# Kernel optimization log

Measured on AMD Instinct MI355X. Metric: run time of the kernel, lower is better.

Reference implementation:

```python
import jax, jax.numpy as jnp
import numpy as np

D_MODEL = 1024
D_QK = 1024
NUM_HEADS = 16
HEAD_DIM = D_QK // NUM_HEADS      # 64
V_DIM = D_MODEL // NUM_HEADS      # 64
B, S = 2, 2048


def setup_inputs() -> dict:
    key = jax.random.key(0)
    ks = jax.random.split(key, 9)
    sc = 0.02
    return {
        "x": jax.random.normal(ks[0], (B, S, D_MODEL), dtype=jnp.float32),
        "Wqk": jax.random.normal(ks[1], (D_MODEL, 2 * D_QK), dtype=jnp.float32) * sc,
        "bqk": jax.random.normal(ks[2], (2 * D_QK,), dtype=jnp.float32) * sc,
        "Wv": jax.random.normal(ks[3], (D_MODEL, D_MODEL), dtype=jnp.float32) * sc,
        "bv": jax.random.normal(ks[4], (D_MODEL,), dtype=jnp.float32) * sc,
        "Wn": jax.random.normal(ks[5], (D_MODEL, NUM_HEADS), dtype=jnp.float32) * sc,
        "bn": jax.random.normal(ks[6], (NUM_HEADS,), dtype=jnp.float32) * sc,
        "Wo": jax.random.normal(ks[7], (D_MODEL, D_MODEL), dtype=jnp.float32) * sc,
        "bo": jax.random.normal(ks[8], (D_MODEL,), dtype=jnp.float32) * sc,
    }


def reference(x, Wqk, bqk, Wv, bv, Wn, bn, Wo, bo):
    b, s, _ = x.shape
    qk = x @ Wqk + bqk                                  # (B,S,2*D_QK)
    v = x @ Wv + bv                                     # (B,S,D_MODEL)
    n = x @ Wn + bn                                     # (B,S,H)

    qk = qk.reshape(b, s, 2, NUM_HEADS, HEAD_DIM)
    q, k = qk[:, :, 0], qk[:, :, 1]                     # (B,S,H,Dh)
    v = v.reshape(b, s, NUM_HEADS, V_DIM)               # (B,S,H,Dv)

    scores = jnp.einsum('bthd,bshd->bhts', q, k)        # (B,H,S,S)
    mask = jnp.tril(jnp.ones((s, s), dtype=scores.dtype))
    n_exp = jnp.exp(jnp.transpose(n, (0, 2, 1)))        # (B,H,S)
    attn = scores * mask / n_exp[:, :, :, None]         # dropout p=0 (eval)

    ctx = jnp.einsum('bhts,bshd->bthd', attn, v)        # (B,S,H,Dv)
    ctx = ctx.reshape(b, s, D_MODEL)
    return ctx @ Wo + bo
```

## Files before the change

kernel.cpp:

```cpp
#include <hip/hip_runtime.h>
#include <hip/hip_bf16.h>

constexpr int Bb   = 2;
constexpr int Ss   = 2048;
constexpr int Dm   = 1024;
constexpr int Hh   = 16;
constexpr int Hd   = 64;
constexpr int Mtot = Bb * Ss;
constexpr int NCH  = Ss / 64;

typedef __bf16 bf16x8 __attribute__((ext_vector_type(8)));
typedef float  f32x4  __attribute__((ext_vector_type(4)));
typedef __attribute__((address_space(1))) unsigned int u32_as1;
typedef __attribute__((address_space(3))) unsigned int u32_as3;

__device__ __forceinline__ void gload_lds16(const void* g, void* l) {
  __builtin_amdgcn_global_load_lds((const u32_as1*)g, (u32_as3*)l, 16, 0, 0);
}

__device__ __forceinline__ unsigned short f2bf(float f) {
  union { float f; unsigned u; } x; x.f = f;
  unsigned r = x.u + 0x7fffu + ((x.u >> 16) & 1u);
  return (unsigned short)(r >> 16);
}

__device__ __forceinline__ float bf2f(unsigned short s) {
  union { unsigned u; float f; } x; x.u = ((unsigned)s) << 16;
  return x.f;
}

__global__ void k_transpose_conv(const float* __restrict__ W, unsigned short* __restrict__ Wt,
                                 int K, int N) {
  __shared__ float t[32][33];
  int n0 = blockIdx.x * 32, k0 = blockIdx.y * 32;
  int tx = threadIdx.x, ty = threadIdx.y;
#pragma unroll
  for (int j = 0; j < 32; j += 8)
    t[ty + j][tx] = W[(size_t)(k0 + ty + j) * N + n0 + tx];
  __syncthreads();
#pragma unroll
  for (int j = 0; j < 32; j += 8)
    Wt[(size_t)(n0 + ty + j) * K + k0 + tx] = f2bf(t[tx][ty + j]);
}

__global__ void k_n_proj(const float* __restrict__ x, const float* __restrict__ Wn,
                         const float* __restrict__ bn, float* __restrict__ invn,
                         unsigned short* __restrict__ xb) {
  __shared__ float xl[4][1024];
  int tid = threadIdx.x, w = tid >> 6, lane = tid & 63;
  int row = blockIdx.x * 4 + w;
  const float4* x4 = (const float4*)(x + (size_t)row * Dm);
  ushort4* xb4 = (ushort4*)(xb + (size_t)row * Dm);
#pragma unroll
  for (int j = 0; j < 4; ++j) {
    float4 v = x4[j * 64 + lane];
    *(float4*)&xl[w][(j * 64 + lane) * 4] = v;
    ushort4 o;
    o.x = f2bf(v.x); o.y = f2bf(v.y); o.z = f2bf(v.z); o.w = f2bf(v.w);
    xb4[j * 64 + lane] = o;
  }
  __syncthreads();
  const float4* Wn4 = (const float4*)Wn;
  f32x4 sum = {0.f, 0.f, 0.f, 0.f};
#pragma unroll 4
  for (int j = 0; j < 64; ++j) {
    float xv = xl[w][j * 16 + (lane >> 2)];
    float4 wv = Wn4[j * 64 + lane];
    sum[0] += xv * wv.x; sum[1] += xv * wv.y; sum[2] += xv * wv.z; sum[3] += xv * wv.w;
  }
#pragma unroll
  for (int m = 4; m < 64; m <<= 1) {
    sum[0] += __shfl_xor(sum[0], m);
    sum[1] += __shfl_xor(sum[1], m);
    sum[2] += __shfl_xor(sum[2], m);
    sum[3] += __shfl_xor(sum[3], m);
  }
  if (lane < 4) {
    int b = row >> 11, s = row & 2047;
#pragma unroll
    for (int e = 0; e < 4; ++e) {
      int h = lane * 4 + e;
      float nv = sum[e] + bn[h];
      invn[((size_t)(b * Hh + h)) * Ss + s] = expf(-nv);
    }
  }
}

template <int MODE>
__global__ __launch_bounds__(256, 2) void k_gemm_bt(
    const unsigned short* __restrict__ A, const unsigned short* __restrict__ BT,
    const float* __restrict__ bias0, const float* __restrict__ bias1,
    void* __restrict__ out0, void* __restrict__ out1, void* __restrict__ out2,
    void* __restrict__ out3, int M, int N, int K) {
  __shared__ __align__(16) unsigned short As[128 * 64];
  __shared__ __align__(16) unsigned short Bs[128 * 64];
  int tid = threadIdx.x, w = tid >> 6, lane = tid & 63;
  int m0 = blockIdx.y * 128, n0 = blockIdx.x * 128;
  int wm = w >> 1, wn = w & 1;
  f32x4 acc[4][4] = {};

  for (int kt = 0; kt < (K >> 6); ++kt) {
#pragma unroll
    for (int i = 0; i < 4; ++i) {
      int lin = i * 2048 + w * 512 + lane * 8;
      int r = lin >> 6, c = lin & 63;
      gload_lds16(A + (size_t)(m0 + r) * K + kt * 64 + c, As + i * 2048 + w * 512);
    }
#pragma unroll
    for (int i = 0; i < 4; ++i) {
      int lin = i * 2048 + w * 512 + lane * 8;
      int r = lin >> 6, c = lin & 63;
      gload_lds16(BT + (size_t)(n0 + r) * K + kt * 64 + c, Bs + i * 2048 + w * 512);
    }
    __syncthreads();
#pragma unroll
    for (int ks = 0; ks < 2; ++ks) {
      bf16x8 af[4], bfr[4];
#pragma unroll
      for (int mt = 0; mt < 4; ++mt)
        af[mt] = *(const bf16x8*)(As + (wm * 64 + mt * 16 + (lane & 15)) * 64 + ks * 32 + (lane >> 4) * 8);
#pragma unroll
      for (int nt = 0; nt < 4; ++nt)
        bfr[nt] = *(const bf16x8*)(Bs + (wn * 64 + nt * 16 + (lane & 15)) * 64 + ks * 32 + (lane >> 4) * 8);
#pragma unroll
      for (int mt = 0; mt < 4; ++mt)
#pragma unroll
        for (int nt = 0; nt < 4; ++nt)
          acc[mt][nt] = __builtin_amdgcn_mfma_f32_16x16x32_bf16(af[mt], bfr[nt], acc[mt][nt], 0, 0, 0);
    }
    __syncthreads();
  }

#pragma unroll
  for (int mt = 0; mt < 4; ++mt) {
#pragma unroll
    for (int nt = 0; nt < 4; ++nt) {
      int n = n0 + wn * 64 + nt * 16 + (lane & 15);
      int tbase = m0 + wm * 64 + mt * 16 + (lane >> 4) * 4;
      if (MODE == 0) {
        int region = n >> 10;
        int h = (n >> 6) & 15, d = n & 63;
        int b = tbase >> 11, t = tbase & 2047;
        float bb = (region < 2) ? bias0[n] : bias1[n - 2048];
        if (region == 0) {
          unsigned short* qp = (unsigned short*)out0;
#pragma unroll
          for (int r = 0; r < 4; ++r)
            qp[(((size_t)(b * Hh + h)) * Ss + t + r) * Hd + d] = f2bf(acc[mt][nt][r] + bb);
        } else if (region == 1) {
          unsigned short* kp = (unsigned short*)out1;
#pragma unroll
          for (int r = 0; r < 4; ++r)
            kp[(((size_t)(b * Hh + h)) * Ss + t + r) * Hd + d] = f2bf(acc[mt][nt][r] + bb);
          ushort4 o;
          o.x = f2bf(acc[mt][nt][0] + bb);
          o.y = f2bf(acc[mt][nt][1] + bb);
          o.z = f2bf(acc[mt][nt][2] + bb);
          o.w = f2bf(acc[mt][nt][3] + bb);
          *(ushort4*)((unsigned short*)out2 + ((size_t)(b * Hh + h) * Hd + d) * Ss + t) = o;
        } else {
          ushort4 o;
          o.x = f2bf(acc[mt][nt][0] + bb);
          o.y = f2bf(acc[mt][nt][1] + bb);
          o.z = f2bf(acc[mt][nt][2] + bb);
          o.w = f2bf(acc[mt][nt][3] + bb);
          *(ushort4*)((unsigned short*)out3 + ((size_t)(b * Hh + h) * Hd + d) * Ss + t) = o;
        }
      } else {
        float bb = bias0[n];
#pragma unroll
        for (int r = 0; r < 4; ++r)
          ((float*)out0)[(size_t)(tbase + r) * N + n] = acc[mt][nt][r] + bb;
      }
    }
  }
}

__global__ __launch_bounds__(64) void k_gram(
    const unsigned short* __restrict__ vT, const unsigned short* __restrict__ kT,
    unsigned short* __restrict__ G) {
  int lane = threadIdx.x;
  int j = blockIdx.x, bh = blockIdx.y;
  int t0 = j * 64;
  const unsigned short* vb = vT + (size_t)bh * Hd * Ss;
  const unsigned short* kb = kT + (size_t)bh * Hd * Ss;
  unsigned short* g = G + ((size_t)bh * NCH + j) * 4096;

  bf16x8 af[4][2], bfr[4][2];
#pragma unroll
  for (int mt = 0; mt < 4; ++mt)
#pragma unroll
    for (int ks = 0; ks < 2; ++ks) {
      af[mt][ks]  = *(const bf16x8*)(vb + (size_t)(mt * 16 + (lane & 15)) * Ss + t0 + ks * 32 + (lane >> 4) * 8);
      bfr[mt][ks] = *(const bf16x8*)(kb + (size_t)(mt * 16 + (lane & 15)) * Ss + t0 + ks * 32 + (lane >> 4) * 8);
    }
  f32x4 acc[4][4] = {};
#pragma unroll
  for (int mt = 0; mt < 4; ++mt)
#pragma unroll
    for (int nt = 0; nt < 4; ++nt)
#pragma unroll
      for (int ks = 0; ks < 2; ++ks)
        acc[mt][nt] = __builtin_amdgcn_mfma_f32_16x16x32_bf16(af[mt][ks], bfr[nt][ks], acc[mt][nt], 0, 0, 0);
#pragma unroll
  for (int mt = 0; mt < 4; ++mt)
#pragma unroll
    for (int nt = 0; nt < 4; ++nt)
#pragma unroll
      for (int r = 0; r < 4; ++r)
        g[(mt * 16 + (lane >> 4) * 4 + r) * 64 + nt * 16 + (lane & 15)] = f2bf(acc[mt][nt][r]);
}

__global__ __launch_bounds__(256) void k_prefix(
    const unsigned short* __restrict__ G, unsigned short* __restrict__ Sp) {
  int gidx = blockIdx.x * 256 + threadIdx.x;
  int bh = gidx >> 12, e = gidx & 4095;
  const unsigned short* gp = G + (size_t)bh * NCH * 4096 + e;
  unsigned short* sp = Sp + (size_t)bh * NCH * 4096 + e;
  float acc = 0.f;
#pragma unroll 8
  for (int j = 0; j < NCH; ++j) {
    sp[(size_t)j * 4096] = f2bf(acc);
    acc += bf2f(gp[(size_t)j * 4096]);
  }
}

__global__ __launch_bounds__(256, 4) void k_chunk_attn(
    const unsigned short* __restrict__ q, const unsigned short* __restrict__ k,
    const unsigned short* __restrict__ vT, const unsigned short* __restrict__ Sp,
    const float* __restrict__ invn, unsigned short* __restrict__ ctx) {
  __shared__ __align__(16) unsigned short P[4 * 16 * 64];
  int tid = threadIdx.x, w = tid >> 6, lane = tid & 63;
  int j = blockIdx.x, bh = blockIdx.y;
  int t0 = j * 64;
  const unsigned short* qb = q + (size_t)bh * Ss * Hd;
  const unsigned short* kb = k + (size_t)bh * Ss * Hd;
  const unsigned short* vb = vT + (size_t)bh * Hd * Ss;
  const unsigned short* sp = Sp + ((size_t)bh * NCH + j) * 4096;

  bf16x8 qf[2];
#pragma unroll
  for (int ks = 0; ks < 2; ++ks)
    qf[ks] = *(const bf16x8*)(qb + (size_t)(t0 + w * 16 + (lane & 15)) * Hd + ks * 32 + (lane >> 4) * 8);

  f32x4 acc[4] = {};
#pragma unroll
  for (int nt = 0; nt < 4; ++nt)
#pragma unroll
    for (int ks = 0; ks < 2; ++ks) {
      bf16x8 sf = *(const bf16x8*)(sp + (nt * 16 + (lane & 15)) * 64 + ks * 32 + (lane >> 4) * 8);
      acc[nt] = __builtin_amdgcn_mfma_f32_16x16x32_bf16(qf[ks], sf, acc[nt], 0, 0, 0);
    }

  f32x4 sacc[4] = {};
#pragma unroll
  for (int nt = 0; nt < 4; ++nt)
#pragma unroll
    for (int ks = 0; ks < 2; ++ks) {
      bf16x8 kf = *(const bf16x8*)(kb + (size_t)(t0 + nt * 16 + (lane & 15)) * Hd + ks * 32 + (lane >> 4) * 8);
      sacc[nt] = __builtin_amdgcn_mfma_f32_16x16x32_bf16(qf[ks], kf, sacc[nt], 0, 0, 0);
    }

#pragma unroll
  for (int nt = 0; nt < 4; ++nt)
#pragma unroll
    for (int r = 0; r < 4; ++r) {
      int row = (lane >> 4) * 4 + r;
      int s_local = nt * 16 + (lane & 15);
      float vv = (s_local <= w * 16 + row) ? sacc[nt][r] : 0.f;
      int cb = s_local * 2;
      int byte = w * 2048 + row * 128 + (cb ^ ((row & 7) << 4));
      *(unsigned short*)((char*)P + byte) = f2bf(vv);
    }
  asm volatile("" ::: "memory");

  bf16x8 pf[2];
#pragma unroll
  for (int ks = 0; ks < 2; ++ks) {
    int prow = lane & 15;
    int pcb = (ks * 32 + (lane >> 4) * 8) * 2;
    pf[ks] = *(const bf16x8*)((char*)P + w * 2048 + prow * 128 + (pcb ^ ((prow & 7) << 4)));
  }
#pragma unroll
  for (int dt = 0; dt < 4; ++dt)
#pragma unroll
    for (int ks = 0; ks < 2; ++ks) {
      bf16x8 vf = *(const bf16x8*)(vb + (size_t)(dt * 16 + (lane & 15)) * Ss + t0 + ks * 32 + (lane >> 4) * 8);
      acc[dt] = __builtin_amdgcn_mfma_f32_16x16x32_bf16(pf[ks], vf, acc[dt], 0, 0, 0);
    }

  int b = bh >> 4, h = bh & 15;
  float sc[4];
#pragma unroll
  for (int r = 0; r < 4; ++r)
    sc[r] = invn[(size_t)bh * Ss + t0 + w * 16 + (lane >> 4) * 4 + r];
#pragma unroll
  for (int dt = 0; dt < 4; ++dt)
#pragma unroll
    for (int r = 0; r < 4; ++r) {
      int t = t0 + w * 16 + (lane >> 4) * 4 + r;
      size_t m = (size_t)b * Ss + t;
      ctx[m * Dm + h * Hd + dt * 16 + (lane & 15)] = f2bf(acc[dt][r] * sc[r]);
    }
}

extern "C" void kernel_launch(void* const* d_in, const int* in_sizes, int n_in,
                              void* d_out, int out_size, void* d_ws, size_t ws_size,
                              hipStream_t stream) {
  const float* x   = (const float*)d_in[0];
  const float* Wqk = (const float*)d_in[1];
  const float* bqk = (const float*)d_in[2];
  const float* Wv  = (const float*)d_in[3];
  const float* bv  = (const float*)d_in[4];
  const float* Wn  = (const float*)d_in[5];
  const float* bn  = (const float*)d_in[6];
  const float* Wo  = (const float*)d_in[7];
  const float* bo  = (const float*)d_in[8];

  char* ws = (char*)d_ws;
  size_t off = 0;
  unsigned short* xb    = (unsigned short*)(ws + off); off += (size_t)Mtot * Dm * 2;
  unsigned short* wprojT= (unsigned short*)(ws + off); off += (size_t)3072 * 1024 * 2;
  unsigned short* woT   = (unsigned short*)(ws + off); off += (size_t)1024 * 1024 * 2;
  unsigned short* qbuf  = (unsigned short*)(ws + off); off += (size_t)Bb * Hh * Ss * Hd * 2;
  unsigned short* kbuf  = (unsigned short*)(ws + off); off += (size_t)Bb * Hh * Ss * Hd * 2;
  unsigned short* ktbuf = (unsigned short*)(ws + off); off += (size_t)Bb * Hh * Ss * Hd * 2;
  unsigned short* vbuf  = (unsigned short*)(ws + off); off += (size_t)Bb * Hh * Ss * Hd * 2;
  float* invn           = (float*)(ws + off);          off += (size_t)Bb * Hh * Ss * 4;
  unsigned short* G     = (unsigned short*)(ws + off); off += (size_t)Bb * Hh * NCH * 4096 * 2;
  unsigned short* Sp    = (unsigned short*)(ws + off); off += (size_t)Bb * Hh * NCH * 4096 * 2;
  unsigned short* ctx   = xb;

  k_transpose_conv<<<dim3(2048 / 32, 1024 / 32), dim3(32, 8), 0, stream>>>(Wqk, wprojT, 1024, 2048);
  k_transpose_conv<<<dim3(1024 / 32, 1024 / 32), dim3(32, 8), 0, stream>>>(Wv, wprojT + (size_t)2048 * 1024, 1024, 1024);
  k_transpose_conv<<<dim3(1024 / 32, 1024 / 32), dim3(32, 8), 0, stream>>>(Wo, woT, 1024, 1024);

  k_n_proj<<<Mtot / 4, 256, 0, stream>>>(x, Wn, bn, invn, xb);

  k_gemm_bt<0><<<dim3(3072 / 128, Mtot / 128), 256, 0, stream>>>(
      xb, wprojT, bqk, bv, qbuf, kbuf, ktbuf, vbuf, Mtot, 3072, 1024);

  k_gram<<<dim3(NCH, Bb * Hh), 64, 0, stream>>>(vbuf, ktbuf, G);
  k_prefix<<<(Bb * Hh * 4096) / 256, 256, 0, stream>>>(G, Sp);
  k_chunk_attn<<<dim3(NCH, Bb * Hh), 256, 0, stream>>>(qbuf, kbuf, vbuf, Sp, invn, ctx);

  k_gemm_bt<2><<<dim3(1024 / 128, Mtot / 128), 256, 0, stream>>>(
      ctx, woT, bo, nullptr, d_out, nullptr, nullptr, nullptr, Mtot, 1024, 1024);
}
```

Before: 119.0 us.

## Replace LDS-staged GEMM with direct global-to-register streaming GEMM and XCD swizzle

The projection and output GEMMs drop LDS staging and barriers. Each wave now loads its MFMA fragments straight from global memory, using a 128x256 block tile where each wave owns 128x64. Block IDs are remapped with an 8-way swizzle to group neighbouring tiles on the same XCD for L2 reuse. This removes shared-memory traffic and syncs, at the cost of redundant A loads across waves, uncoalesced strided global reads, and fewer blocks for the output GEMM.

New measurement: 213.4 us. 1.79x slower.

```diff
diff --git a/kernel.cpp b/kernel.cpp
--- a/kernel.cpp
+++ b/kernel.cpp
@@ -11,12 +11,6 @@
 
 typedef __bf16 bf16x8 __attribute__((ext_vector_type(8)));
 typedef float  f32x4  __attribute__((ext_vector_type(4)));
-typedef __attribute__((address_space(1))) unsigned int u32_as1;
-typedef __attribute__((address_space(3))) unsigned int u32_as3;
-
-__device__ __forceinline__ void gload_lds16(const void* g, void* l) {
-  __builtin_amdgcn_global_load_lds((const u32_as1*)g, (u32_as3*)l, 16, 0, 0);
-}
 
 __device__ __forceinline__ unsigned short f2bf(float f) {
   union { float f; unsigned u; } x; x.f = f;
@@ -86,57 +80,50 @@
   }
 }
 
-template <int MODE>
-__global__ __launch_bounds__(256, 2) void k_gemm_bt(
+template <int MODE, int Nn, int Kk>
+__global__ __launch_bounds__(256, 2) void k_gemm_stream(
     const unsigned short* __restrict__ A, const unsigned short* __restrict__ BT,
     const float* __restrict__ bias0, const float* __restrict__ bias1,
-    void* __restrict__ out0, void* __restrict__ out1, void* __restrict__ out2,
-    void* __restrict__ out3, int M, int N, int K) {
-  __shared__ __align__(16) unsigned short As[128 * 64];
-  __shared__ __align__(16) unsigned short Bs[128 * 64];
+    void* __restrict__ out0, void* __restrict__ out1,
+    void* __restrict__ out2, void* __restrict__ out3) {
   int tid = threadIdx.x, w = tid >> 6, lane = tid & 63;
-  int m0 = blockIdx.y * 128, n0 = blockIdx.x * 128;
-  int wm = w >> 1, wn = w & 1;
-  f32x4 acc[4][4] = {};
-
-  for (int kt = 0; kt < (K >> 6); ++kt) {
-#pragma unroll
-    for (int i = 0; i < 4; ++i) {
-      int lin = i * 2048 + w * 512 + lane * 8;
-      int r = lin >> 6, c = lin & 63;
-      gload_lds16(A + (size_t)(m0 + r) * K + kt * 64 + c, As + i * 2048 + w * 512);
-    }
-#pragma unroll
-    for (int i = 0; i < 4; ++i) {
-      int lin = i * 2048 + w * 512 + lane * 8;
-      int r = lin >> 6, c = lin & 63;
-      gload_lds16(BT + (size_t)(n0 + r) * K + kt * 64 + c, Bs + i * 2048 + w * 512);
-    }
-    __syncthreads();
-#pragma unroll
-    for (int ks = 0; ks < 2; ++ks) {
-      bf16x8 af[4], bfr[4];
-#pragma unroll
-      for (int mt = 0; mt < 4; ++mt)
-        af[mt] = *(const bf16x8*)(As + (wm * 64 + mt * 16 + (lane & 15)) * 64 + ks * 32 + (lane >> 4) * 8);
-#pragma unroll
-      for (int nt = 0; nt < 4; ++nt)
-        bfr[nt] = *(const bf16x8*)(Bs + (wn * 64 + nt * 16 + (lane & 15)) * 64 + ks * 32 + (lane >> 4) * 8);
-#pragma unroll
-      for (int mt = 0; mt < 4; ++mt)
-#pragma unroll
-        for (int nt = 0; nt < 4; ++nt)
-          acc[mt][nt] = __builtin_amdgcn_mfma_f32_16x16x32_bf16(af[mt], bfr[nt], acc[mt][nt], 0, 0, 0);
-    }
-    __syncthreads();
-  }
-
-#pragma unroll
-  for (int mt = 0; mt < 4; ++mt) {
-#pragma unroll
-    for (int nt = 0; nt < 4; ++nt) {
-      int n = n0 + wn * 64 + nt * 16 + (lane & 15);
-      int tbase = m0 + wm * 64 + mt * 16 + (lane >> 4) * 4;
+  int gx = gridDim.x, gy = gridDim.y;
+  int nwg = gx * gy;
+  int bid = blockIdx.y * gx + blockIdx.x;
+  int cpx = nwg >> 3;
+  int swz = (bid & 7) * cpx + (bid >> 3);
+  int bx = swz / gy, by = swz - bx * gy;
+  int m0 = by * 128;
+  int n0 = bx * 256 + w * 64;
+
+  const unsigned short* Ab = A  + (size_t)(m0 + (lane & 15)) * Kk + (lane >> 4) * 8;
+  const unsigned short* Bb = BT + (size_t)(n0 + (lane & 15)) * Kk + (lane >> 4) * 8;
+
+  f32x4 acc[8][4] = {};
+  for (int kt = 0; kt < (Kk >> 6); ++kt) {
+#pragma unroll
+    for (int ks = 0; ks < 2; ++ks) {
+      bf16x8 af[8], bfr[4];
+#pragma unroll
+      for (int mf = 0; mf < 8; ++mf)
+        af[mf] = *(const bf16x8*)(Ab + (size_t)mf * 16 * Kk + kt * 64 + ks * 32);
+#pragma unroll
+      for (int nf = 0; nf < 4; ++nf)
+        bfr[nf] = *(const bf16x8*)(Bb + (size_t)nf * 16 * Kk + kt * 64 + ks * 32);
+#pragma unroll
+      for (int mf = 0; mf < 8; ++mf)
+#pragma unroll
+        for (int nf = 0; nf < 4; ++nf)
+          acc[mf][nf] = __builtin_amdgcn_mfma_f32_16x16x32_bf16(af[mf], bfr[nf], acc[mf][nf], 0, 0, 0);
+    }
+  }
+
+#pragma unroll
+  for (int mf = 0; mf < 8; ++mf) {
+#pragma unroll
+    for (int nf = 0; nf < 4; ++nf) {
+      int n = n0 + nf * 16 + (lane & 15);
+      int tbase = m0 + mf * 16 + (lane >> 4) * 4;
       if (MODE == 0) {
         int region = n >> 10;
         int h = (n >> 6) & 15, d = n & 63;
@@ -146,31 +133,31 @@
           unsigned short* qp = (unsigned short*)out0;
 #pragma unroll
           for (int r = 0; r < 4; ++r)
-            qp[(((size_t)(b * Hh + h)) * Ss + t + r) * Hd + d] = f2bf(acc[mt][nt][r] + bb);
+            qp[(((size_t)(b * Hh + h)) * Ss + t + r) * Hd + d] = f2bf(acc[mf][nf][r] + bb);
         } else if (region == 1) {
           unsigned short* kp = (unsigned short*)out1;
 #pragma unroll
           for (int r = 0; r < 4; ++r)
-            kp[(((size_t)(b * Hh + h)) * Ss + t + r) * Hd + d] = f2bf(acc[mt][nt][r] + bb);
+            kp[(((size_t)(b * Hh + h)) * Ss + t + r) * Hd + d] = f2bf(acc[mf][nf][r] + bb);
           ushort4 o;
-          o.x = f2bf(acc[mt][nt][0] + bb);
-          o.y = f2bf(acc[mt][nt][1] + bb);
-          o.z = f2bf(acc[mt][nt][2] + bb);
-          o.w = f2bf(acc[mt][nt][3] + bb);
+          o.x = f2bf(acc[mf][nf][0] + bb);
+          o.y = f2bf(acc[mf][nf][1] + bb);
+          o.z = f2bf(acc[mf][nf][2] + bb);
+          o.w = f2bf(acc[mf][nf][3] + bb);
           *(ushort4*)((unsigned short*)out2 + ((size_t)(b * Hh + h) * Hd + d) * Ss + t) = o;
         } else {
           ushort4 o;
-          o.x = f2bf(acc[mt][nt][0] + bb);
-          o.y = f2bf(acc[mt][nt][1] + bb);
-          o.z = f2bf(acc[mt][nt][2] + bb);
-          o.w = f2bf(acc[mt][nt][3] + bb);
+          o.x = f2bf(acc[mf][nf][0] + bb);
+          o.y = f2bf(acc[mf][nf][1] + bb);
+          o.z = f2bf(acc[mf][nf][2] + bb);
+          o.w = f2bf(acc[mf][nf][3] + bb);
           *(ushort4*)((unsigned short*)out3 + ((size_t)(b * Hh + h) * Hd + d) * Ss + t) = o;
         }
       } else {
         float bb = bias0[n];
 #pragma unroll
         for (int r = 0; r < 4; ++r)
-          ((float*)out0)[(size_t)(tbase + r) * N + n] = acc[mt][nt][r] + bb;
+          ((float*)out0)[(size_t)(tbase + r) * Nn + n] = acc[mf][nf][r] + bb;
       }
     }
   }
@@ -337,13 +324,13 @@
 
   k_n_proj<<<Mtot / 4, 256, 0, stream>>>(x, Wn, bn, invn, xb);
 
-  k_gemm_bt<0><<<dim3(3072 / 128, Mtot / 128), 256, 0, stream>>>(
-      xb, wprojT, bqk, bv, qbuf, kbuf, ktbuf, vbuf, Mtot, 3072, 1024);
+  k_gemm_stream<0, 3072, 1024><<<dim3(3072 / 256, Mtot / 128), 256, 0, stream>>>(
+      xb, wprojT, bqk, bv, qbuf, kbuf, ktbuf, vbuf);
 
   k_gram<<<dim3(NCH, Bb * Hh), 64, 0, stream>>>(vbuf, ktbuf, G);
   k_prefix<<<(Bb * Hh * 4096) / 256, 256, 0, stream>>>(G, Sp);
   k_chunk_attn<<<dim3(NCH, Bb * Hh), 256, 0, stream>>>(qbuf, kbuf, vbuf, Sp, invn, ctx);
 
-  k_gemm_bt<2><<<dim3(1024 / 128, Mtot / 128), 256, 0, stream>>>(
-      ctx, woT, bo, nullptr, d_out, nullptr, nullptr, nullptr, Mtot, 1024, 1024);
-}
+  k_gemm_stream<2, 1024, 1024><<<dim3(1024 / 256, Mtot / 128), 256, 0, stream>>>(
+      ctx, woT, bo, nullptr, d_out, nullptr, nullptr, nullptr);
+}
```
